# Kernel tuning notes

Hardware: AMD Instinct MI355X
Metric: run time of the kernel (lower is better)

The kernel has to match this reference:

```python
import jax, jax.numpy as jnp
import numpy as np

NUM_FREQS = 10  # 3 coords * 10 freqs * (sin, cos) = 60 channels


def posencode3(pos):
    """NeRF-style positional encoding. pos: (B, 3, N) -> (B, 60, N)."""
    freqs = (2.0 ** jnp.arange(NUM_FREQS, dtype=pos.dtype))  # (F,)
    x = pos[:, :, None, :] * freqs[None, None, :, None]      # (B, 3, F, N)
    emb = jnp.concatenate([jnp.sin(x), jnp.cos(x)], axis=2)  # (B, 3, 2F, N)
    B, _, _, N = emb.shape
    return emb.reshape(B, 3 * 2 * NUM_FREQS, N)              # (B, 60, N)


def setup_inputs() -> dict:
    key = jax.random.key(0)
    ks = jax.random.split(key, 7)
    B, N, DIM, C = 8, 2048, 384, 60
    return {
        "pos": jax.random.normal(ks[0], (B, 3, N), dtype=jnp.float32),
        "Wq": jax.random.normal(ks[1], (DIM, C), dtype=jnp.float32) * 0.05,
        "bq": jax.random.normal(ks[2], (DIM,), dtype=jnp.float32) * 0.05,
        "Wk": jax.random.normal(ks[3], (DIM, C), dtype=jnp.float32) * 0.05,
        "bk": jax.random.normal(ks[4], (DIM,), dtype=jnp.float32) * 0.05,
        "Wv": jax.random.normal(ks[5], (DIM, C), dtype=jnp.float32) * 0.05,
        "bv": jax.random.normal(ks[6], (DIM,), dtype=jnp.float32) * 0.05,
    }


def reference(pos, Wq, bq, Wk, bk, Wv, bv):
    dim = Wq.shape[0]
    scale = dim ** (-0.5)
    pe = posencode3(pos)                                   # (B, 60, N)
    # Conv1d(kernel=1) == pointwise matmul over channel dim
    q = jnp.einsum('dc,bcn->bdn', Wq, pe) + bq[None, :, None]
    k = jnp.einsum('dc,bcn->bdn', Wk, pe) + bk[None, :, None]
    v = jnp.einsum('dc,bcn->bdn', Wv, pe) + bv[None, :, None]
    # Faithful to source: attn = (q^T @ k) / scale, scale = dim**-0.5
    attn = jnp.einsum('bdn,bdm->bnm', q, k) / scale        # (B, N, N)
    attn = jax.nn.softmax(attn, axis=-1)
    out = jnp.einsum('bnm,bdm->bdn', attn, v)              # (B, dim, N)
    return out
```

## Files before the change

### kernel.cpp

```cpp
#include <hip/hip_runtime.h>
#include <stdint.h>


typedef unsigned short u16;
typedef unsigned int   u32;
using h16x8 = __attribute__((ext_vector_type(8))) _Float16;
using f32x4 = __attribute__((ext_vector_type(4))) float;

#define MF16(a,b,c) __builtin_amdgcn_mfma_f32_16x16x32_f16((a),(b),(c),0,0,0)

__device__ __forceinline__ u16 f2h_u(float x) { union { _Float16 h; u16 u; } v; v.h = (_Float16)x; return v.u; }
__device__ __forceinline__ float h2f(u16 u)   { union { _Float16 h; u16 u; } v; v.u = u; return (float)v.h; }

__device__ __forceinline__ float rmax16(float x) {
  x = fmaxf(x, __shfl_xor(x, 1, 16));
  x = fmaxf(x, __shfl_xor(x, 2, 16));
  x = fmaxf(x, __shfl_xor(x, 4, 16));
  x = fmaxf(x, __shfl_xor(x, 8, 16));
  return x;
}

__device__ __forceinline__ void glds16(const void* g, u16* l) {
  __builtin_amdgcn_global_load_lds((const __attribute__((address_space(1))) u32*)g,
                                   (__attribute__((address_space(3))) u32*)l, 16, 0, 0);
}

#define QH_OFF 0u
#define QL_OFF 12582912u
#define KH_OFF 25165824u
#define VV_OFF 37748736u

#define SC 28.270933952f

#define PH_E 0
#define PL_E 4608
#define WH_E 9216
#define WL_E 23040
#define TT_E 9216

__global__ __launch_bounds__(256, 2) void qkv_kernel(
    const float* __restrict__ pos,
    const float* __restrict__ Wq, const float* __restrict__ bq,
    const float* __restrict__ Wk, const float* __restrict__ bk,
    const float* __restrict__ Wv, const float* __restrict__ bv,
    u16* __restrict__ qh, u16* __restrict__ ql,
    u16* __restrict__ kh, u16* __restrict__ vv)
{
  const int tid = threadIdx.x;
  const int b = blockIdx.x & 7, nt = (blockIdx.x >> 3) & 31, h = blockIdx.x >> 8;
  const int w = tid >> 6, q15 = tid & 15, quad = (tid & 63) >> 4;

  __shared__ __align__(16) u16 sm[36864];

  if (tid < 192) {
    const int coord = tid >> 6, n = tid & 63;
    const float p = pos[(b * 3 + coord) * 2048 + nt * 64 + n];
    const int base = n * 72 + coord * 20;
    u16 sh[10], ch[10], sl[10], cl[10];
#pragma unroll
    for (int j = 0; j < 10; ++j) {
      float x = p * (float)(1 << j);
      float s = __sinf(x), c = __cosf(x);
      sh[j] = f2h_u(s); sl[j] = f2h_u(s - h2f(sh[j]));
      ch[j] = f2h_u(c); cl[j] = f2h_u(c - h2f(ch[j]));
    }
#pragma unroll
    for (int j = 0; j < 10; j += 2) {
      *(u32*)&sm[PH_E + base + j]      = (u32)sh[j] | ((u32)sh[j + 1] << 16);
      *(u32*)&sm[PH_E + base + 10 + j] = (u32)ch[j] | ((u32)ch[j + 1] << 16);
      *(u32*)&sm[PL_E + base + j]      = (u32)sl[j] | ((u32)sl[j + 1] << 16);
      *(u32*)&sm[PL_E + base + 10 + j] = (u32)cl[j] | ((u32)cl[j + 1] << 16);
    }
  } else {
    const int n = tid - 192;
#pragma unroll
    for (int j = 0; j < 12; j += 2) {
      *(u32*)&sm[PH_E + n * 72 + 60 + j] = 0;
      *(u32*)&sm[PL_E + n * 72 + 60 + j] = 0;
    }
  }

  for (int mat = 0; mat < 3; ++mat) {
    const float* Wg = (mat == 0) ? Wq : ((mat == 1) ? Wk : Wv);
    const float* bg = (mat == 0) ? bq : ((mat == 1) ? bk : bv);
    __syncthreads();

    for (int i = tid; i < 2880; i += 256) {
      float4 v = *(const float4*)&Wg[(size_t)h * 11520 + (size_t)i * 4];
      int dd = i / 15, c4 = i % 15;
      int base = dd * 72 + c4 * 4;
      u16 h0 = f2h_u(v.x), h1 = f2h_u(v.y), h2 = f2h_u(v.z), h3 = f2h_u(v.w);
      ushort4 hv; hv.x = h0; hv.y = h1; hv.z = h2; hv.w = h3;
      ushort4 lv;
      lv.x = f2h_u(v.x - h2f(h0)); lv.y = f2h_u(v.y - h2f(h1));
      lv.z = f2h_u(v.z - h2f(h2)); lv.w = f2h_u(v.w - h2f(h3));
      *(ushort4*)&sm[WH_E + base] = hv;
      *(ushort4*)&sm[WL_E + base] = lv;
    }
    for (int i = tid; i < 2304; i += 256) {
      int dd = i / 12, c = 60 + i % 12;
      sm[WH_E + dd * 72 + c] = 0;
      sm[WL_E + dd * 72 + c] = 0;
    }
    __syncthreads();

    f32x4 acc[3][4];
#pragma unroll
    for (int rf = 0; rf < 3; ++rf)
#pragma unroll
      for (int nf = 0; nf < 4; ++nf) acc[rf][nf] = (f32x4){0.f, 0.f, 0.f, 0.f};

#pragma unroll
    for (int ks = 0; ks < 2; ++ks) {
      const int co = ks * 32 + quad * 8;
      h16x8 bh[4], bl[4];
#pragma unroll
      for (int nf = 0; nf < 4; ++nf) {
        bh[nf] = *(const h16x8*)&sm[PH_E + (nf * 16 + q15) * 72 + co];
        bl[nf] = *(const h16x8*)&sm[PL_E + (nf * 16 + q15) * 72 + co];
      }
#pragma unroll
      for (int rf = 0; rf < 3; ++rf) {
        h16x8 ah = *(const h16x8*)&sm[WH_E + (w * 48 + rf * 16 + q15) * 72 + co];
        h16x8 al = *(const h16x8*)&sm[WL_E + (w * 48 + rf * 16 + q15) * 72 + co];
#pragma unroll
        for (int nf = 0; nf < 4; ++nf) {
          acc[rf][nf] = MF16(ah, bh[nf], acc[rf][nf]);
          acc[rf][nf] = MF16(ah, bl[nf], acc[rf][nf]);
          acc[rf][nf] = MF16(al, bh[nf], acc[rf][nf]);
        }
      }
    }

#pragma unroll
    for (int rf = 0; rf < 3; ++rf)
#pragma unroll
      for (int r = 0; r < 4; ++r) {
        float bi = bg[h * 192 + w * 48 + rf * 16 + quad * 4 + r];
#pragma unroll
        for (int nf = 0; nf < 4; ++nf) {
          float v = acc[rf][nf][r] + bi;
          acc[rf][nf][r] = (mat == 0) ? v * SC : v;
        }
      }
    __syncthreads();

    if (mat == 2) {
#pragma unroll
      for (int rf = 0; rf < 3; ++rf)
#pragma unroll
        for (int nf = 0; nf < 4; ++nf)
#pragma unroll
          for (int r = 0; r < 4; ++r)
            sm[TT_E + (w * 48 + rf * 16 + quad * 4 + r) * 72 + nf * 16 + q15] = f2h_u(acc[rf][nf][r]);
      __syncthreads();
      for (int c = tid; c < 1536; c += 256) {
        int d = c >> 3, k = c & 7;
        *(uint4*)&vv[((size_t)(b * 384 + h * 192 + d)) * 2048 + nt * 64 + k * 8] =
            *(const uint4*)&sm[TT_E + d * 72 + k * 8];
      }
    } else {
      const int npass = (mat == 0) ? 2 : 1;
      for (int pass = 0; pass < npass; ++pass) {
#pragma unroll
        for (int rf = 0; rf < 3; ++rf)
#pragma unroll
          for (int nf = 0; nf < 4; ++nf) {
            u16 e[4];
#pragma unroll
            for (int r = 0; r < 4; ++r) {
              float v = acc[rf][nf][r];
              e[r] = (pass == 0) ? f2h_u(v) : f2h_u(v - h2f(f2h_u(v)));
            }
            ushort4 pv; pv.x = e[0]; pv.y = e[1]; pv.z = e[2]; pv.w = e[3];
            *(ushort4*)&sm[TT_E + (nf * 16 + q15) * 200 + w * 48 + rf * 16 + quad * 4] = pv;
          }
        __syncthreads();
        u16* dst = (mat == 1) ? kh : ((pass == 0) ? qh : ql);
        for (int c = tid; c < 1536; c += 256) {
          int n = c / 24, k = c % 24;
          *(uint4*)&dst[((size_t)(b * 2048 + nt * 64 + n)) * 384 + h * 192 + k * 8] =
              *(const uint4*)&sm[TT_E + n * 200 + k * 8];
        }
        if (pass + 1 < npass) __syncthreads();
      }
    }
  }
}

#define KEH(kh,f) ((kh) * 24576 + (f) * 12288)
#define VEH(kh)   (49152 + (kh) * 12800)
#define PEH       74752
#define K2_LDS_BYTES 159744

__global__ __launch_bounds__(512) __attribute__((amdgpu_waves_per_eu(2))) void attn_kernel(
    const u16* __restrict__ qhp, const u16* __restrict__ qlp,
    const u16* __restrict__ khp, const u16* __restrict__ vvp,
    float* __restrict__ outp)
{
  extern __shared__ __align__(16) u16 smem[];
  const int tid = threadIdx.x;
  const int b = blockIdx.x & 7, qt = blockIdx.x >> 3;
  const int w = tid >> 6, lane = tid & 63, q15 = lane & 15, quad = lane >> 4;
  const int kh2 = w >> 2, qw = w & 3;

  int kfo[6];
#pragma unroll
  for (int j = 0; j < 3; ++j)
#pragma unroll
    for (int p = 0; p < 2; ++p) {
      int sub = j * 1024 + lane * 16;
      int r0 = sub / 768;
      int cp = (sub - r0 * 768) >> 4;
      int rx = (4 * p + r0) & 7;
      int cl = (cp & ~7) | ((cp & 7) ^ rx);
      kfo[j * 2 + p] = r0 * 768 + cl * 16;
    }

  h16x8 qfh[12], qfl[12];
  {
    const size_t qr = ((size_t)(b * 2048 + qt * 64 + qw * 16 + q15)) * 384;
#pragma unroll
    for (int ks = 0; ks < 12; ++ks) {
      qfh[ks] = *(const h16x8*)&qhp[qr + ks * 32 + quad * 8];
      qfl[ks] = *(const h16x8*)&qlp[qr + ks * 32 + quad * 8];
    }
  }

  for (int i = tid; i < 1024; i += 512) {
    int half = i >> 9, rr = (i >> 5) & 15, cc = i & 31;
    smem[VEH(half) + (384 + rr) * 32 + cc] = (rr == 0) ? (u16)0x3C00 : (u16)0;
  }

  const char* kbase = (const char*)(khp + ((size_t)b * 2048 + kh2 * 1024) * 384);

#pragma unroll
  for (int t = 0; t < 6; ++t) {
    int g = qw * 2 + t / 3;
    glds16(kbase + g * 3072 + kfo[(t % 3) * 2 + (g & 1)],
           &smem[KEH(kh2, 0) + (qw * 6 + t) * 512]);
  }
  __syncthreads();

  f32x4 o[25];
#pragma unroll
  for (int cf = 0; cf < 25; ++cf) o[cf] = (f32x4){0.f, 0.f, 0.f, 0.f};
  float mo[4];
#pragma unroll
  for (int r = 0; r < 4; ++r) mo[r] = -1e30f;

  for (int mt = 0; mt < 32; ++mt) {
    const int cur = mt & 1;

    {
      const char* vt = (const char*)(vvp + (size_t)b * 384 * 2048 + kh2 * 1024 + mt * 32);
#pragma unroll
      for (int t = 0; t < 6; ++t) {
        int i = qw * 6 + t;
        int d = i * 16 + (lane >> 2), s = lane & 3;
        glds16(vt + (size_t)d * 4096 + ((s ^ (d & 3)) * 16), &smem[VEH(kh2) + i * 512]);
      }
    }
    {
      const char* kt = kbase + ((mt + 1) & 31) * 32 * 768;
#pragma unroll
      for (int t = 0; t < 6; ++t) {
        int g = qw * 2 + t / 3;
        glds16(kt + g * 3072 + kfo[(t % 3) * 2 + (g & 1)],
               &smem[KEH(kh2, cur ^ 1) + (qw * 6 + t) * 512]);
      }
    }

    f32x4 sa[2], sb[2];
#pragma unroll
    for (int cf = 0; cf < 2; ++cf) { sa[cf] = (f32x4){0.f,0.f,0.f,0.f}; sb[cf] = (f32x4){0.f,0.f,0.f,0.f}; }
#pragma unroll
    for (int ks = 0; ks < 12; ++ks) {
#pragma unroll
      for (int cf = 0; cf < 2; ++cf) {
        const int row = cf * 16 + q15;
        const int c3 = (((ks & 1) * 4) | quad) ^ (q15 & 7);
        h16x8 bk = *(const h16x8*)&smem[KEH(kh2, cur) + row * 384 + ((ks >> 1) * 8 + c3) * 8];
        sa[cf] = MF16(qfh[ks], bk, sa[cf]);
        sb[cf] = MF16(qfl[ks], bk, sb[cf]);
      }
    }
#pragma unroll
    for (int cf = 0; cf < 2; ++cf) sa[cf] += sb[cf];

    float al[4], p0[4], p1[4];
#pragma unroll
    for (int r = 0; r < 4; ++r) {
      float mx = rmax16(fmaxf(sa[0][r], sa[1][r]));
      float mn = fmaxf(mo[r], mx);
      al[r] = exp2f(mo[r] - mn);
      mo[r] = mn;
      p0[r] = exp2f(sa[0][r] - mn);
      p1[r] = exp2f(sa[1][r] - mn);
    }
#pragma unroll
    for (int r = 0; r < 4; ++r) {
      smem[PEH + w * 640 + (quad * 4 + r) * 40 +      q15] = f2h_u(p0[r]);
      smem[PEH + w * 640 + (quad * 4 + r) * 40 + 16 + q15] = f2h_u(p1[r]);
    }
#pragma unroll
    for (int cf = 0; cf < 25; ++cf)
#pragma unroll
      for (int r = 0; r < 4; ++r) o[cf][r] *= al[r];

    __syncthreads();

    h16x8 pa = *(const h16x8*)&smem[PEH + w * 640 + q15 * 40 + quad * 8];
#pragma unroll
    for (int cf = 0; cf < 25; ++cf) {
      const int d = cf * 16 + q15;
      h16x8 vb = *(const h16x8*)&smem[VEH(kh2) + d * 32 + ((quad ^ (d & 3)) * 8)];
      o[cf] = MF16(pa, vb, o[cf]);
    }

    __syncthreads();
  }

  float* M  = (float*)smem;
  float* Lm = M + 26112;
  float* Ll = M + 26176;

  if (kh2 == 1) {
#pragma unroll
    for (int cf = 0; cf < 24; ++cf) {
      float4 st; st.x = o[cf][0]; st.y = o[cf][1]; st.z = o[cf][2]; st.w = o[cf][3];
      *(float4*)&M[(size_t)(cf * 16 + q15) * 68 + qw * 16 + quad * 4] = st;
    }
    if (q15 == 0) {
#pragma unroll
      for (int r = 0; r < 4; ++r) {
        Lm[qw * 16 + quad * 4 + r] = mo[r];
        Ll[qw * 16 + quad * 4 + r] = o[24][r];
      }
    }
  }
  __syncthreads();

  if (kh2 == 0) {
    float eA[4], eB[4], inv[4];
#pragma unroll
    for (int r = 0; r < 4; ++r) {
      const int n = qw * 16 + quad * 4 + r;
      float lA = __shfl(o[24][r], 0, 16);
      float mB = Lm[n], lB = Ll[n];
      float mn = fmaxf(mo[r], mB);
      eA[r] = exp2f(mo[r] - mn);
      eB[r] = exp2f(mB - mn);
      inv[r] = 1.0f / (lA * eA[r] + lB * eB[r]);
    }
#pragma unroll
    for (int cf = 0; cf < 24; ++cf) {
      const int d = cf * 16 + q15;
      float4 ob = *(const float4*)&M[(size_t)d * 68 + qw * 16 + quad * 4];
      float4 st;
      st.x = (o[cf][0] * eA[0] + ob.x * eB[0]) * inv[0];
      st.y = (o[cf][1] * eA[1] + ob.y * eB[1]) * inv[1];
      st.z = (o[cf][2] * eA[2] + ob.z * eB[2]) * inv[2];
      st.w = (o[cf][3] * eA[3] + ob.w * eB[3]) * inv[3];
      *(float4*)&outp[((size_t)(b * 384 + d)) * 2048 + qt * 64 + qw * 16 + quad * 4] = st;
    }
  }
}

extern "C" void kernel_launch(void* const* d_in, const int* in_sizes, int n_in,
                              void* d_out, int out_size, void* d_ws, size_t ws_size,
                              hipStream_t stream) {
  const float* pos = (const float*)d_in[0];
  const float* Wq  = (const float*)d_in[1];
  const float* bq  = (const float*)d_in[2];
  const float* Wk  = (const float*)d_in[3];
  const float* bk  = (const float*)d_in[4];
  const float* Wv  = (const float*)d_in[5];
  const float* bv  = (const float*)d_in[6];

  char* ws = (char*)d_ws;
  u16* qh = (u16*)(ws + QH_OFF);
  u16* ql = (u16*)(ws + QL_OFF);
  u16* kh = (u16*)(ws + KH_OFF);
  u16* vv = (u16*)(ws + VV_OFF);

  qkv_kernel<<<512, 256, 0, stream>>>(pos, Wq, bq, Wk, bk, Wv, bv, qh, ql, kh, vv);
  attn_kernel<<<256, 512, K2_LDS_BYTES, stream>>>(qh, ql, kh, vv, (float*)d_out);
}
```

Baseline: 263.1 us.

## Drop split-KV within attention block; each block of 4 waves scans all keys

The attention kernel previously split the 2048 keys into two halves processed by two groups of 4 waves, then merged partial softmax states through LDS. Now each 256-thread block iterates over all 64 key tiles itself, removing the cross-half merge, its LDS staging and the extra barrier, and halving the LDS footprint. In exchange, each block runs twice as many serial iterations with half the waves, so per-CU parallelism and latency hiding drop unless occupancy rises from the smaller LDS use.

```diff
diff --git a/kernel.cpp b/kernel.cpp
--- a/kernel.cpp
+++ b/kernel.cpp
@@ -188,12 +188,12 @@
   }
 }
 
-#define KEH(kh,f) ((kh) * 24576 + (f) * 12288)
-#define VEH(kh)   (49152 + (kh) * 12800)
-#define PEH       74752
-#define K2_LDS_BYTES 159744
-
-__global__ __launch_bounds__(512) __attribute__((amdgpu_waves_per_eu(2))) void attn_kernel(
+#define KE2(f) ((f) * 12288)
+#define VE2    24576
+#define PE2    37376
+#define K2_LDS_BYTES 79872
+
+__global__ __launch_bounds__(256) __attribute__((amdgpu_waves_per_eu(2))) void attn_kernel(
     const u16* __restrict__ qhp, const u16* __restrict__ qlp,
     const u16* __restrict__ khp, const u16* __restrict__ vvp,
     float* __restrict__ outp)
@@ -202,7 +202,6 @@
   const int tid = threadIdx.x;
   const int b = blockIdx.x & 7, qt = blockIdx.x >> 3;
   const int w = tid >> 6, lane = tid & 63, q15 = lane & 15, quad = lane >> 4;
-  const int kh2 = w >> 2, qw = w & 3;
 
   int kfo[6];
 #pragma unroll
@@ -219,7 +218,7 @@
 
   h16x8 qfh[12], qfl[12];
   {
-    const size_t qr = ((size_t)(b * 2048 + qt * 64 + qw * 16 + q15)) * 384;
+    const size_t qr = ((size_t)(b * 2048 + qt * 64 + w * 16 + q15)) * 384;
 #pragma unroll
     for (int ks = 0; ks < 12; ++ks) {
       qfh[ks] = *(const h16x8*)&qhp[qr + ks * 32 + quad * 8];
@@ -227,18 +226,18 @@
     }
   }
 
-  for (int i = tid; i < 1024; i += 512) {
-    int half = i >> 9, rr = (i >> 5) & 15, cc = i & 31;
-    smem[VEH(half) + (384 + rr) * 32 + cc] = (rr == 0) ? (u16)0x3C00 : (u16)0;
-  }
-
-  const char* kbase = (const char*)(khp + ((size_t)b * 2048 + kh2 * 1024) * 384);
+  for (int i = tid; i < 512; i += 256) {
+    int rr = (i >> 5) & 15, cc = i & 31;
+    smem[VE2 + (384 + rr) * 32 + cc] = (rr == 0) ? (u16)0x3C00 : (u16)0;
+  }
+
+  const char* kbase = (const char*)(khp + (size_t)b * 2048 * 384);
 
 #pragma unroll
   for (int t = 0; t < 6; ++t) {
-    int g = qw * 2 + t / 3;
+    int g = w * 2 + t / 3;
     glds16(kbase + g * 3072 + kfo[(t % 3) * 2 + (g & 1)],
-           &smem[KEH(kh2, 0) + (qw * 6 + t) * 512]);
+           &smem[KE2(0) + (w * 6 + t) * 512]);
   }
   __syncthreads();
 
@@ -249,25 +248,25 @@
 #pragma unroll
   for (int r = 0; r < 4; ++r) mo[r] = -1e30f;
 
-  for (int mt = 0; mt < 32; ++mt) {
+  for (int mt = 0; mt < 64; ++mt) {
     const int cur = mt & 1;
 
     {
-      const char* vt = (const char*)(vvp + (size_t)b * 384 * 2048 + kh2 * 1024 + mt * 32);
+      const char* vt = (const char*)(vvp + (size_t)b * 384 * 2048 + mt * 32);
 #pragma unroll
       for (int t = 0; t < 6; ++t) {
-        int i = qw * 6 + t;
+        int i = w * 6 + t;
         int d = i * 16 + (lane >> 2), s = lane & 3;
-        glds16(vt + (size_t)d * 4096 + ((s ^ (d & 3)) * 16), &smem[VEH(kh2) + i * 512]);
+        glds16(vt + (size_t)d * 4096 + ((s ^ (d & 3)) * 16), &smem[VE2 + i * 512]);
       }
     }
     {
-      const char* kt = kbase + ((mt + 1) & 31) * 32 * 768;
+      const char* kt = kbase + ((mt + 1) & 63) * 32 * 768;
 #pragma unroll
       for (int t = 0; t < 6; ++t) {
-        int g = qw * 2 + t / 3;
+        int g = w * 2 + t / 3;
         glds16(kt + g * 3072 + kfo[(t % 3) * 2 + (g & 1)],
-               &smem[KEH(kh2, cur ^ 1) + (qw * 6 + t) * 512]);
+               &smem[KE2(cur ^ 1) + (w * 6 + t) * 512]);
       }
     }
 
@@ -280,7 +279,7 @@
       for (int cf = 0; cf < 2; ++cf) {
         const int row = cf * 16 + q15;
         const int c3 = (((ks & 1) * 4) | quad) ^ (q15 & 7);
-        h16x8 bk = *(const h16x8*)&smem[KEH(kh2, cur) + row * 384 + ((ks >> 1) * 8 + c3) * 8];
+        h16x8 bk = *(const h16x8*)&smem[KE2(cur) + row * 384 + ((ks >> 1) * 8 + c3) * 8];
         sa[cf] = MF16(qfh[ks], bk, sa[cf]);
         sb[cf] = MF16(qfl[ks], bk, sb[cf]);
       }
@@ -300,8 +299,8 @@
     }
 #pragma unroll
     for (int r = 0; r < 4; ++r) {
-      smem[PEH + w * 640 + (quad * 4 + r) * 40 +      q15] = f2h_u(p0[r]);
-      smem[PEH + w * 640 + (quad * 4 + r) * 40 + 16 + q15] = f2h_u(p1[r]);
+      smem[PE2 + w * 640 + (quad * 4 + r) * 40 +      q15] = f2h_u(p0[r]);
+      smem[PE2 + w * 640 + (quad * 4 + r) * 40 + 16 + q15] = f2h_u(p1[r]);
     }
 #pragma unroll
     for (int cf = 0; cf < 25; ++cf)
@@ -310,60 +309,28 @@
 
     __syncthreads();
 
-    h16x8 pa = *(const h16x8*)&smem[PEH + w * 640 + q15 * 40 + quad * 8];
+    h16x8 pa = *(const h16x8*)&smem[PE2 + w * 640 + q15 * 40 + quad * 8];
 #pragma unroll
     for (int cf = 0; cf < 25; ++cf) {
       const int d = cf * 16 + q15;
-      h16x8 vb = *(const h16x8*)&smem[VEH(kh2) + d * 32 + ((quad ^ (d & 3)) * 8)];
+      h16x8 vb = *(const h16x8*)&smem[VE2 + d * 32 + ((quad ^ (d & 3)) * 8)];
       o[cf] = MF16(pa, vb, o[cf]);
     }
 
     __syncthreads();
   }
 
-  float* M  = (float*)smem;
-  float* Lm = M + 26112;
-  float* Ll = M + 26176;
-
-  if (kh2 == 1) {
-#pragma unroll
-    for (int cf = 0; cf < 24; ++cf) {
-      float4 st; st.x = o[cf][0]; st.y = o[cf][1]; st.z = o[cf][2]; st.w = o[cf][3];
-      *(float4*)&M[(size_t)(cf * 16 + q15) * 68 + qw * 16 + quad * 4] = st;
-    }
-    if (q15 == 0) {
-#pragma unroll
-      for (int r = 0; r < 4; ++r) {
-        Lm[qw * 16 + quad * 4 + r] = mo[r];
-        Ll[qw * 16 + quad * 4 + r] = o[24][r];
-      }
-    }
-  }
-  __syncthreads();
-
-  if (kh2 == 0) {
-    float eA[4], eB[4], inv[4];
-#pragma unroll
-    for (int r = 0; r < 4; ++r) {
-      const int n = qw * 16 + quad * 4 + r;
-      float lA = __shfl(o[24][r], 0, 16);
-      float mB = Lm[n], lB = Ll[n];
-      float mn = fmaxf(mo[r], mB);
-      eA[r] = exp2f(mo[r] - mn);
-      eB[r] = exp2f(mB - mn);
-      inv[r] = 1.0f / (lA * eA[r] + lB * eB[r]);
-    }
-#pragma unroll
-    for (int cf = 0; cf < 24; ++cf) {
-      const int d = cf * 16 + q15;
-      float4 ob = *(const float4*)&M[(size_t)d * 68 + qw * 16 + quad * 4];
-      float4 st;
-      st.x = (o[cf][0] * eA[0] + ob.x * eB[0]) * inv[0];
-      st.y = (o[cf][1] * eA[1] + ob.y * eB[1]) * inv[1];
-      st.z = (o[cf][2] * eA[2] + ob.z * eB[2]) * inv[2];
-      st.w = (o[cf][3] * eA[3] + ob.w * eB[3]) * inv[3];
-      *(float4*)&outp[((size_t)(b * 384 + d)) * 2048 + qt * 64 + qw * 16 + quad * 4] = st;
-    }
+  float inv[4];
+#pragma unroll
+  for (int r = 0; r < 4; ++r)
+    inv[r] = 1.0f / __shfl(o[24][r], 0, 16);
+#pragma unroll
+  for (int cf = 0; cf < 24; ++cf) {
+    const int d = cf * 16 + q15;
+    float4 st;
+    st.x = o[cf][0] * inv[0]; st.y = o[cf][1] * inv[1];
+    st.z = o[cf][2] * inv[2]; st.w = o[cf][3] * inv[3];
+    *(float4*)&outp[((size_t)(b * 384 + d)) * 2048 + qt * 64 + w * 16 + quad * 4] = st;
   }
 }
 
@@ -385,5 +352,5 @@
   u16* vv = (u16*)(ws + VV_OFF);
 
   qkv_kernel<<<512, 256, 0, stream>>>(pos, Wq, bq, Wk, bk, Wv, bv, qh, ql, kh, vv);
-  attn_kernel<<<256, 512, K2_LDS_BYTES, stream>>>(qh, ql, kh, vv, (float*)d_out);
-}
+  attn_kernel<<<256, 256, K2_LDS_BYTES, stream>>>(qh, ql, kh, vv, (float*)d_out);
+}
```

After: 436.0 us. 1.66x slower.
